# Kernel optimization log

Measured on AMD Instinct MI355X. Metric: run time of the kernel, lower is better.

## Reference

```python
import jax, jax.numpy as jnp
import numpy as np

B, L, N, F = 8, 4096, 128, 128          # batch, pixels (64x64), memories, filters
H, DK, DV = 8, 16, 32                   # heads, key dim/head, value dim/head
TK, TV = H * DK, H * DV                 # total key depth 128, total value depth 256
BOT, FFN = 256, 2048                    # bottleneck (2*filters), feed-forward channels
EPS = 1e-3                              # keras BatchNormalization epsilon
INV = float(1.0 / np.sqrt(1.0 + EPS))   # inference BN with moving mean=0, var=1


def _bn_pair(k, shape):
    kg, kb = jax.random.split(k)
    gamma = jax.random.uniform(kg, shape, jnp.float32, 0.5, 1.5)
    beta = 0.1 * jax.random.normal(kb, shape, jnp.float32)
    return jnp.stack([gamma, beta])


def setup_inputs() -> dict:
    key = jax.random.key(0)
    ks = jax.random.split(key, 24)
    s = float(BOT) ** -0.5  # TruncatedNormal(stddev=bottleneck**-0.5) init for qkv convs
    return {
        "pixel_input": jax.random.normal(ks[0], (B, L, F), jnp.float32),
        "memory_input": jax.random.normal(ks[1], (B, N, F), jnp.float32),
        "W_mem1": 0.05 * jax.random.normal(ks[2], (F, BOT), jnp.float32),
        "bn_mem1": _bn_pair(ks[3], (BOT,)),
        "W_pix1": 0.05 * jax.random.normal(ks[4], (F, BOT), jnp.float32),
        "bn_pix1": _bn_pair(ks[5], (BOT,)),
        "W_mem_qkv": s * jax.random.normal(ks[6], (BOT, 2 * TK + TV), jnp.float32),
        "bn_mem_qkv": _bn_pair(ks[7], (2 * TK + TV,)),
        "W_pix_qkv": s * jax.random.normal(ks[8], (BOT, 2 * TK + TV), jnp.float32),
        "bn_pix_qkv": _bn_pair(ks[9], (2 * TK + TV,)),
        "bn_mem_sim": _bn_pair(ks[10], (H,)),
        "bn_mem_ret": _bn_pair(ks[11], (H, DV)),
        "bn_pix_sim": _bn_pair(ks[12], (H,)),
        "bn_pix_ret": _bn_pair(ks[13], (H, DV)),
        "W_mem3": 0.05 * jax.random.normal(ks[14], (TV, F), jnp.float32),
        "bn_mem3": _bn_pair(ks[15], (F,)),
        "W_pix3": 0.05 * jax.random.normal(ks[16], (TV, F), jnp.float32),
        "bn_pix3": _bn_pair(ks[17], (F,)),
        "W_ffn1": 0.05 * jax.random.normal(ks[18], (F, FFN), jnp.float32),
        "bn_ffn1": _bn_pair(ks[19], (FFN,)),
        "W_ffn2": 0.05 * jax.random.normal(ks[20], (FFN, F), jnp.float32),
        "bn_ffn2": _bn_pair(ks[21], (F,)),
    }


def _cbn(x, W, p, relu=False):
    """Conv1D (kernel=1) + inference BatchNorm over channels (+ optional relu)."""
    y = jnp.einsum('blc,cd->bld', x, W)
    y = y * (p[0] * INV) + p[1]
    return jax.nn.relu(y) if relu else y


def _heads(t, d):
    b, l, _ = t.shape  # [b, l, H*d] -> [b, H, l, d]
    return t.reshape(b, l, H, d).transpose(0, 2, 1, 3)


def reference(pixel_input, memory_input, W_mem1, bn_mem1, W_pix1, bn_pix1,
              W_mem_qkv, bn_mem_qkv, W_pix_qkv, bn_pix_qkv,
              bn_mem_sim, bn_mem_ret, bn_pix_sim, bn_pix_ret,
              W_mem3, bn_mem3, W_pix3, bn_pix3,
              W_ffn1, bn_ffn1, W_ffn2, bn_ffn2):
    # Bottleneck projections (conv1 + BN + relu)
    mem = _cbn(memory_input, W_mem1, bn_mem1, True)   # [B, N, BOT]
    pix = _cbn(pixel_input, W_pix1, bn_pix1, True)    # [B, L, BOT]

    # QKV projections (conv + BN, no activation)
    mqkv = _cbn(mem, W_mem_qkv, bn_mem_qkv)           # [B, N, 2*TK+TV]
    pqkv = _cbn(pix, W_pix_qkv, bn_pix_qkv)           # [B, L, 2*TK+TV]
    mq, mk, mv = mqkv[..., :TK], mqkv[..., TK:2 * TK], mqkv[..., 2 * TK:]
    pq, pk, pv = pqkv[..., :TK], pqkv[..., TK:2 * TK], pqkv[..., 2 * TK:]
    mq_h, mk_h = _heads(mq, DK), _heads(mk, DK)       # [B, H, N, DK]
    pq_h, pk_h = _heads(pq, DK), _heads(pk, DK)       # [B, H, L, DK]
    mv_h = mv.reshape(B, N, H, DV)                    # [B, N, H, DV]
    pv_h = pv.reshape(B, L, H, DV)                    # [B, L, H, DV]

    # Memory path: memory2pixel attention + memory self-attention share softmax
    k_cat = jnp.concatenate([pk_h, mk_h], axis=2)     # [B, H, L+N, DK]
    v_cat = jnp.concatenate([pv_h, mv_h], axis=1)     # [B, L+N, H, DV]
    logits = jnp.einsum('bhnd,bhmd->bhnm', mq_h, k_cat)
    logits = logits * (bn_mem_sim[0] * INV)[None, :, None, None] + bn_mem_sim[1][None, :, None, None]
    attn = jax.nn.softmax(logits, axis=-1)
    ret = jnp.einsum('bhnm,bmhd->bhnd', attn, v_cat)  # [B, H, N, DV]
    ret = ret * (bn_mem_ret[0] * INV)[None, :, None, :] + bn_mem_ret[1][None, :, None, :]
    ret = jax.nn.relu(ret).transpose(0, 2, 1, 3).reshape(B, N, TV)
    mem_out = jax.nn.relu(memory_input + _cbn(ret, W_mem3, bn_mem3))
    ffn = _cbn(mem_out, W_ffn1, bn_ffn1, True)
    mem_out = jax.nn.relu(mem_out + _cbn(ffn, W_ffn2, bn_ffn2))

    # Pixel path: pixel2memory feedback attention (sigmoid activation)
    plogits = jnp.einsum('bhld,bhnd->bhln', pq_h, mk_h)
    plogits = plogits * (bn_pix_sim[0] * INV)[None, :, None, None] + bn_pix_sim[1][None, :, None, None]
    pattn = jax.nn.sigmoid(plogits)
    pret = jnp.einsum('bhln,bnhd->bhld', pattn, mv_h)  # [B, H, L, DV]
    pret = pret * (bn_pix_ret[0] * INV)[None, :, None, :] + bn_pix_ret[1][None, :, None, :]
    pret = jax.nn.relu(pret).transpose(0, 2, 1, 3).reshape(B, L, TV)
    pix_out = jax.nn.relu(pixel_input + _cbn(pret, W_pix3, bn_pix3))

    return pix_out, mem_out
```

## Files before the change

### kernel.cpp

```cpp
#include <hip/hip_runtime.h>

typedef __attribute__((ext_vector_type(8))) short short8;
typedef __attribute__((ext_vector_type(4))) float floatx4;

#define INVC 0.9995003746877732f
#define MSPLIT 8

__device__ __forceinline__ unsigned short f2bf(float f) {
    union { float f; unsigned int u; } c; c.f = f;
    unsigned int r = c.u + 0x7fffu + ((c.u >> 16) & 1u);
    return (unsigned short)(r >> 16);
}
__device__ __forceinline__ float bf2f(unsigned short u) {
    union { unsigned int u; float f; } c; c.u = ((unsigned int)u) << 16;
    return c.f;
}
__device__ __forceinline__ void gld_lds16(const unsigned short* g, unsigned short* l) {
    __builtin_amdgcn_global_load_lds(
        (const __attribute__((address_space(1))) unsigned int*)g,
        (__attribute__((address_space(3))) unsigned int*)l, 16, 0, 0);
}
__device__ __forceinline__ int fidx(int row, int k) {
    return (k >> 5) * 512 + (row + 16 * ((k >> 3) & 3)) * 8 + (k & 7);
}

struct PrepPtrs {
    const float* src_pix;
    unsigned short* dst_pix;
    const float* W[8]; unsigned short* Wt[8];
};

__global__ __launch_bounds__(256) void prep_kernel(PrepPtrs P) {
    __shared__ float T[32][33];
    const int bid = blockIdx.x, t = threadIdx.x;
    if (bid < 4096) {
        int i = bid * 1024 + t * 4;
        float4 v = *(const float4*)(P.src_pix + i);
        unsigned long long pk = (unsigned long long)f2bf(v.x)
            | ((unsigned long long)f2bf(v.y) << 16)
            | ((unsigned long long)f2bf(v.z) << 32)
            | ((unsigned long long)f2bf(v.w) << 48);
        *(unsigned long long*)(P.dst_pix + i) = pk;
        return;
    }
    int rel = bid - 4096;
    const int KD[8]  = {128,128,256,256,256,256,128,2048};
    const int ND[8]  = {256,256,512,512,128,128,2048,128};
    const int CNT[8] = {32,32,128,128,32,32,256,256};
    int wi = 0;
    #pragma unroll
    for (int k = 0; k < 8; ++k) { if (rel >= CNT[k] && wi == k) { rel -= CNT[k]; wi = k + 1; } }
    const int K = KD[wi], N = ND[wi];
    const int ntn = N >> 5;
    const int tn = rel % ntn, tk = rel / ntn;
    const int n0 = tn * 32, k0 = tk * 32;
    const float* W = P.W[wi];
    unsigned short* Wt = P.Wt[wi];
    const int tx = t & 31, ty = t >> 5;
    #pragma unroll
    for (int i = 0; i < 4; ++i)
        T[ty + 8*i][tx] = W[(size_t)(k0 + ty + 8*i) * N + n0 + tx];
    __syncthreads();
    #pragma unroll
    for (int i = 0; i < 4; ++i)
        Wt[(size_t)(n0 + ty + 8*i) * K + k0 + tx] = f2bf(T[tx][ty + 8*i]);
}

__global__ __launch_bounds__(256, 4) void gemm_bf16(
    const unsigned short* __restrict__ A,
    const unsigned short* __restrict__ Bt,
    const float* __restrict__ bnp,
    const float* __restrict__ residF,
    unsigned short* __restrict__ outB,
    float* __restrict__ outF,
    int M, int K, int Nc, int do_relu)
{
    __shared__ unsigned short As[8 * 512];
    __shared__ unsigned short Bs[8 * 512];
    const int t = threadIdx.x;
    const int lane = t & 63, w = t >> 6;
    const int l15 = lane & 15, quad = lane >> 4;
    const int wr = w >> 1, wc = w & 1;
    const int row0 = blockIdx.y * 128;
    const int col0 = blockIdx.x * 128;

    floatx4 acc[4][4];
    #pragma unroll
    for (int i = 0; i < 4; ++i)
        #pragma unroll
        for (int j = 0; j < 4; ++j) acc[i][j] = (floatx4){0.f, 0.f, 0.f, 0.f};

    const unsigned short* gA0 = A  + (size_t)(row0 + w*16     + l15) * K + quad*8;
    const unsigned short* gA1 = A  + (size_t)(row0 + (w+4)*16 + l15) * K + quad*8;
    const unsigned short* gB0 = Bt + (size_t)(col0 + w*16     + l15) * K + quad*8;
    const unsigned short* gB1 = Bt + (size_t)(col0 + (w+4)*16 + l15) * K + quad*8;
    unsigned short* lA0 = &As[w * 512];
    unsigned short* lA1 = &As[(w + 4) * 512];
    unsigned short* lB0 = &Bs[w * 512];
    unsigned short* lB1 = &Bs[(w + 4) * 512];

    for (int k0 = 0; k0 < K; k0 += 32) {
        __syncthreads();
        gld_lds16(gA0 + k0, lA0);
        gld_lds16(gA1 + k0, lA1);
        gld_lds16(gB0 + k0, lB0);
        gld_lds16(gB1 + k0, lB1);
        __syncthreads();
        short8 a[4], b[4];
        #pragma unroll
        for (int mt = 0; mt < 4; ++mt) a[mt] = *(const short8*)&As[(wr*4 + mt)*512 + lane*8];
        #pragma unroll
        for (int nt = 0; nt < 4; ++nt) b[nt] = *(const short8*)&Bs[(wc*4 + nt)*512 + lane*8];
        #pragma unroll
        for (int mt = 0; mt < 4; ++mt)
            #pragma unroll
            for (int nt = 0; nt < 4; ++nt)
                acc[mt][nt] = __builtin_amdgcn_mfma_f32_16x16x32_bf16(a[mt], b[nt], acc[mt][nt], 0, 0, 0);
    }

    #pragma unroll
    for (int mt = 0; mt < 4; ++mt) {
        const int rowb = row0 + wr*64 + mt*16 + quad*4;
        #pragma unroll
        for (int nt = 0; nt < 4; ++nt) {
            const int col = col0 + wc*64 + nt*16 + l15;
            floatx4 v = acc[mt][nt];
            const float g  = bnp[col] * INVC;
            const float be = bnp[Nc + col];
            #pragma unroll
            for (int r = 0; r < 4; ++r) {
                size_t off = (size_t)(rowb + r) * Nc + col;
                float v1 = v[r] * g + be;
                if (residF) v1 += residF[off];
                if (do_relu) v1 = fmaxf(v1, 0.f);
                if (outB) outB[off] = f2bf(v1);
                if (outF) outF[off] = v1;
            }
        }
    }
}

__global__ __launch_bounds__(256) void mem_fused(
    const float* __restrict__ memory_input,
    const unsigned short* __restrict__ Wt0, const float* __restrict__ bn1,
    const unsigned short* __restrict__ Wt2, const float* __restrict__ bnq,
    unsigned short* __restrict__ mqkv)
{
    __shared__ unsigned short A0[4*512];
    __shared__ unsigned short A1[8*512];
    const int t = threadIdx.x;
    const int lane = t & 63, w = t >> 6;
    const int l15 = lane & 15, quad = lane >> 4;
    const int g0 = blockIdx.x * 16;

    {
        const int row = t >> 4;
        const int c0 = (t & 15) * 8;
        const float* src = memory_input + (size_t)(g0 + row) * 128 + c0;
        float4 v0 = *(const float4*)src;
        float4 v1 = *(const float4*)(src + 4);
        float vv[8] = {v0.x, v0.y, v0.z, v0.w, v1.x, v1.y, v1.z, v1.w};
        #pragma unroll
        for (int e = 0; e < 8; ++e)
            A0[fidx(row, c0 + e)] = f2bf(vv[e]);
    }
    __syncthreads();

    #pragma unroll
    for (int i = 0; i < 4; ++i) {
        const int n0 = (w*4 + i) * 16;
        floatx4 acc = {0.f,0.f,0.f,0.f};
        #pragma unroll
        for (int kc = 0; kc < 4; ++kc) {
            short8 a = *(const short8*)&A0[kc*512 + lane*8];
            short8 bfr = *(const short8*)&Wt0[(size_t)(n0 + l15)*128 + kc*32 + quad*8];
            acc = __builtin_amdgcn_mfma_f32_16x16x32_bf16(a, bfr, acc, 0, 0, 0);
        }
        const int col = n0 + l15;
        const float g = bn1[col] * INVC, be = bn1[256 + col];
        #pragma unroll
        for (int r = 0; r < 4; ++r) {
            const int row = quad*4 + r;
            float v = fmaxf(acc[r]*g + be, 0.f);
            A1[fidx(row, col)] = f2bf(v);
        }
    }
    __syncthreads();

    #pragma unroll
    for (int i = 0; i < 8; ++i) {
        const int n0 = w*128 + i*16;
        floatx4 acc = {0.f,0.f,0.f,0.f};
        #pragma unroll
        for (int kc = 0; kc < 8; ++kc) {
            short8 a = *(const short8*)&A1[kc*512 + lane*8];
            short8 bfr = *(const short8*)&Wt2[(size_t)(n0 + l15)*256 + kc*32 + quad*8];
            acc = __builtin_amdgcn_mfma_f32_16x16x32_bf16(a, bfr, acc, 0, 0, 0);
        }
        const int col = n0 + l15;
        const float g = bnq[col] * INVC, be = bnq[512 + col];
        #pragma unroll
        for (int r = 0; r < 4; ++r) {
            const int row = quad*4 + r;
            mqkv[(size_t)(g0 + row)*512 + col] = f2bf(acc[r]*g + be);
        }
    }
}

__global__ __launch_bounds__(256) void ffn_fused(
    const float* __restrict__ part_acc, const float* __restrict__ part_ml,
    const float* __restrict__ bn_ret,
    const unsigned short* __restrict__ Wt4, const float* __restrict__ bn3,
    const float* __restrict__ memory_input,
    const unsigned short* __restrict__ Wt6, const float* __restrict__ bnf1,
    const unsigned short* __restrict__ Wt7, const float* __restrict__ bnf2,
    float* __restrict__ out_mem)
{
    __shared__ unsigned short mretA[8*512];
    __shared__ unsigned short moA[4*512];
    __shared__ unsigned short fA[64*512];
    const int t = threadIdx.x;
    const int lane = t & 63, w = t >> 6;
    const int l15 = lane & 15, quad = lane >> 4;
    const int g0 = blockIdx.x * 16;
    const int b = g0 >> 7;
    const int nbase = g0 & 127;

    {
        const int row = t >> 4;
        const int c0 = (t & 15) * 16;
        const int h = c0 >> 5;
        const int n = nbase + row;
        const int bh = b*8 + h;
        float ms[MSPLIT], ls[MSPLIT], m_g = -1e30f;
        #pragma unroll
        for (int s = 0; s < MSPLIT; ++s) {
            size_t o = ((size_t)(bh*MSPLIT + s)*128 + n)*2;
            ms[s] = part_ml[o]; ls[s] = part_ml[o+1];
            m_g = fmaxf(m_g, ms[s]);
        }
        float l_g = 0.f;
        float og[16];
        #pragma unroll
        for (int e = 0; e < 16; ++e) og[e] = 0.f;
        #pragma unroll
        for (int s = 0; s < MSPLIT; ++s) {
            float wgt = __expf(ms[s] - m_g);
            l_g += ls[s] * wgt;
            const float* pa = part_acc + ((size_t)(bh*MSPLIT + s)*128 + n)*32 + (c0 & 31);
            #pragma unroll
            for (int e = 0; e < 16; e += 4) {
                float4 v = *(const float4*)(pa + e);
                og[e]   += v.x*wgt; og[e+1] += v.y*wgt;
                og[e+2] += v.z*wgt; og[e+3] += v.w*wgt;
            }
        }
        float invl = 1.f / l_g;
        #pragma unroll
        for (int e = 0; e < 16; ++e) {
            int col = c0 + e;
            int dv = col & 31;
            float v = og[e]*invl*(bn_ret[h*32+dv]*INVC) + bn_ret[256 + h*32 + dv];
            mretA[fidx(row, col)] = f2bf(fmaxf(v, 0.f));
        }
    }
    __syncthreads();

    floatx4 mo[2];
    #pragma unroll
    for (int i = 0; i < 2; ++i) {
        const int n0 = (w*2 + i) * 16;
        floatx4 acc = {0.f,0.f,0.f,0.f};
        #pragma unroll
        for (int kc = 0; kc < 8; ++kc) {
            short8 a = *(const short8*)&mretA[kc*512 + lane*8];
            short8 bfr = *(const short8*)&Wt4[(size_t)(n0 + l15)*256 + kc*32 + quad*8];
            acc = __builtin_amdgcn_mfma_f32_16x16x32_bf16(a, bfr, acc, 0, 0, 0);
        }
        const int col = n0 + l15;
        const float g = bn3[col]*INVC, be = bn3[128 + col];
        #pragma unroll
        for (int r = 0; r < 4; ++r) {
            const int row = quad*4 + r;
            float v = acc[r]*g + be + memory_input[(size_t)(g0 + row)*128 + col];
            v = fmaxf(v, 0.f);
            mo[i][r] = v;
            moA[fidx(row, col)] = f2bf(v);
        }
    }
    __syncthreads();

    for (int nt = 0; nt < 32; ++nt) {
        const int n0 = w*512 + nt*16;
        floatx4 acc = {0.f,0.f,0.f,0.f};
        #pragma unroll
        for (int kc = 0; kc < 4; ++kc) {
            short8 a = *(const short8*)&moA[kc*512 + lane*8];
            short8 bfr = *(const short8*)&Wt6[(size_t)(n0 + l15)*128 + kc*32 + quad*8];
            acc = __builtin_amdgcn_mfma_f32_16x16x32_bf16(a, bfr, acc, 0, 0, 0);
        }
        const int col = n0 + l15;
        const float g = bnf1[col]*INVC, be = bnf1[2048 + col];
        #pragma unroll
        for (int r = 0; r < 4; ++r) {
            const int row = quad*4 + r;
            fA[fidx(row, col)] = f2bf(fmaxf(acc[r]*g + be, 0.f));
        }
    }
    __syncthreads();

    #pragma unroll
    for (int i = 0; i < 2; ++i) {
        const int n0 = (w*2 + i) * 16;
        floatx4 acc = {0.f,0.f,0.f,0.f};
        #pragma unroll 8
        for (int kc = 0; kc < 64; ++kc) {
            short8 a = *(const short8*)&fA[kc*512 + lane*8];
            short8 bfr = *(const short8*)&Wt7[(size_t)(n0 + l15)*2048 + kc*32 + quad*8];
            acc = __builtin_amdgcn_mfma_f32_16x16x32_bf16(a, bfr, acc, 0, 0, 0);
        }
        const int col = n0 + l15;
        const float g = bnf2[col]*INVC, be = bnf2[128 + col];
        #pragma unroll
        for (int r = 0; r < 4; ++r) {
            const int row = quad*4 + r;
            float v = fmaxf(acc[r]*g + be + mo[i][r], 0.f);
            out_mem[(size_t)(g0 + row)*128 + col] = v;
        }
    }
}

__global__ __launch_bounds__(256) void pix_attn(
    const unsigned short* __restrict__ pqkv,
    const unsigned short* __restrict__ mqkv,
    const float* __restrict__ bn_sim,
    const float* __restrict__ bn_ret,
    unsigned short* __restrict__ pret)
{
    __shared__ unsigned short Qs[128][40];
    __shared__ unsigned short Ks[128][40];
    __shared__ unsigned short VsT[32][136];
    __shared__ unsigned short Ps[128][136];
    const int t = threadIdx.x;
    const int lane = t & 63, w = t >> 6;
    const int l15 = lane & 15, quad = lane >> 4;
    const int bx = blockIdx.x;
    const int lt = bx & 31, h = (bx >> 5) & 7, b = bx >> 8;
    const int l0 = lt * 128;
    const float simg = bn_sim[h] * INVC, simb = bn_sim[8 + h];

    {
        const int r = t >> 1, half = t & 1;
        uint4 zz = make_uint4(0u, 0u, 0u, 0u);
        const unsigned short* qsrc = pqkv + ((size_t)(b*4096 + l0 + r) << 9) + h*16 + half*8;
        *(uint4*)&Qs[r][half*8] = *(const uint4*)qsrc;
        *(uint4*)&Qs[r][16 + half*8] = zz;
        const unsigned short* ksrc = mqkv + ((size_t)(b*128 + r) << 9) + 128 + h*16 + half*8;
        *(uint4*)&Ks[r][half*8] = *(const uint4*)ksrc;
        *(uint4*)&Ks[r][16 + half*8] = zz;
        const unsigned short* vsrc = mqkv + ((size_t)(b*128 + r) << 9) + 256 + h*32 + half*16;
        uint4 va = *(const uint4*)vsrc;
        uint4 vb = *(const uint4*)(vsrc + 8);
        const int d0 = half * 16;
        VsT[d0+0][r] = (unsigned short)(va.x & 0xffffu); VsT[d0+1][r] = (unsigned short)(va.x >> 16);
        VsT[d0+2][r] = (unsigned short)(va.y & 0xffffu); VsT[d0+3][r] = (unsigned short)(va.y >> 16);
        VsT[d0+4][r] = (unsigned short)(va.z & 0xffffu); VsT[d0+5][r] = (unsigned short)(va.z >> 16);
        VsT[d0+6][r] = (unsigned short)(va.w & 0xffffu); VsT[d0+7][r] = (unsigned short)(va.w >> 16);
        VsT[d0+8][r] = (unsigned short)(vb.x & 0xffffu); VsT[d0+9][r] = (unsigned short)(vb.x >> 16);
        VsT[d0+10][r] = (unsigned short)(vb.y & 0xffffu); VsT[d0+11][r] = (unsigned short)(vb.y >> 16);
        VsT[d0+12][r] = (unsigned short)(vb.z & 0xffffu); VsT[d0+13][r] = (unsigned short)(vb.z >> 16);
        VsT[d0+14][r] = (unsigned short)(vb.w & 0xffffu); VsT[d0+15][r] = (unsigned short)(vb.w >> 16);
    }
    __syncthreads();

    floatx4 z4 = {0.f, 0.f, 0.f, 0.f};
    #pragma unroll
    for (int half = 0; half < 2; ++half) {
        short8 aq = *(const short8*)&Qs[w*32 + half*16 + l15][quad*8];
        #pragma unroll
        for (int nt = 0; nt < 8; ++nt) {
            short8 bk = *(const short8*)&Ks[nt*16 + l15][quad*8];
            floatx4 s = __builtin_amdgcn_mfma_f32_16x16x32_bf16(aq, bk, z4, 0, 0, 0);
            const int rowb = w*32 + half*16 + quad*4;
            #pragma unroll
            for (int r = 0; r < 4; ++r) {
                float x = s[r] * simg + simb;
                float p = 1.f / (1.f + __expf(-x));
                Ps[rowb + r][nt*16 + l15] = f2bf(p);
            }
        }
    }
    __syncthreads();

    #pragma unroll
    for (int half = 0; half < 2; ++half) {
        const int mrow = w*32 + half*16;
        #pragma unroll
        for (int dvt = 0; dvt < 2; ++dvt) {
            floatx4 acc = {0.f, 0.f, 0.f, 0.f};
            #pragma unroll
            for (int ks = 0; ks < 4; ++ks) {
                short8 ap = *(const short8*)&Ps[mrow + l15][ks*32 + quad*8];
                short8 bv = *(const short8*)&VsT[dvt*16 + l15][ks*32 + quad*8];
                acc = __builtin_amdgcn_mfma_f32_16x16x32_bf16(ap, bv, acc, 0, 0, 0);
            }
            const int dv = dvt*16 + l15;
            const float g  = bn_ret[h*32 + dv] * INVC;
            const float be = bn_ret[256 + h*32 + dv];
            #pragma unroll
            for (int r = 0; r < 4; ++r) {
                const int row = l0 + mrow + quad*4 + r;
                float v = fmaxf(acc[r] * g + be, 0.f);
                pret[((size_t)(b*4096 + row) << 8) + h*32 + dv] = f2bf(v);
            }
        }
    }
}

__global__ __launch_bounds__(256) void mem_attn(
    const unsigned short* __restrict__ mqkv,
    const unsigned short* __restrict__ pqkv,
    const float* __restrict__ bn_sim,
    float* __restrict__ part_acc,
    float* __restrict__ part_ml)
{
    __shared__ unsigned short Qs[128][40];
    __shared__ unsigned short Ks[128][40];
    __shared__ unsigned short VsT[32][136];
    __shared__ unsigned short Ps[128][136];
    const int t = threadIdx.x;
    const int lane = t & 63, w = t >> 6;
    const int l15 = lane & 15, quad = lane >> 4;
    const int bx = blockIdx.x;
    const int s = bx & (MSPLIT-1), h = (bx >> 3) & 7, b = bx >> 6;
    const int bh = b*8 + h;
    const float simg = bn_sim[h] * INVC, simb = bn_sim[8 + h];
    const int c0  = (s == 0) ? 0 : (4*s + 1);
    const int cnt = (s == 0) ? 5 : 4;

    {
        const int r = t >> 1, half = t & 1;
        uint4 zz = make_uint4(0u, 0u, 0u, 0u);
        const unsigned short* qsrc = mqkv + ((size_t)(b*128 + r) << 9) + h*16 + half*8;
        *(uint4*)&Qs[r][half*8] = *(const uint4*)qsrc;
        *(uint4*)&Qs[r][16 + half*8] = zz;
    }

    float m_run[2][4], l_run[2][4];
    floatx4 accpv[2][2];
    #pragma unroll
    for (int i = 0; i < 2; ++i) {
        #pragma unroll
        for (int r = 0; r < 4; ++r) { m_run[i][r] = -1e30f; l_run[i][r] = 0.f; }
        accpv[i][0] = (floatx4){0.f,0.f,0.f,0.f};
        accpv[i][1] = (floatx4){0.f,0.f,0.f,0.f};
    }
    floatx4 z4 = {0.f, 0.f, 0.f, 0.f};

    for (int ci = 0; ci < cnt; ++ci) {
        const int c = c0 + ci;
        __syncthreads();
        {
            const int r = t >> 1, half = t & 1;
            uint4 zz = make_uint4(0u, 0u, 0u, 0u);
            const unsigned short* base = (c < 32)
                ? (pqkv + ((size_t)(b*4096 + c*128 + r) << 9))
                : (mqkv + ((size_t)(b*128 + r) << 9));
            *(uint4*)&Ks[r][half*8] = *(const uint4*)(base + 128 + h*16 + half*8);
            *(uint4*)&Ks[r][16 + half*8] = zz;
            const unsigned short* vsrc = base + 256 + h*32 + half*16;
            uint4 va = *(const uint4*)vsrc;
            uint4 vb = *(const uint4*)(vsrc + 8);
            const int d0 = half * 16;
            VsT[d0+0][r] = (unsigned short)(va.x & 0xffffu); VsT[d0+1][r] = (unsigned short)(va.x >> 16);
            VsT[d0+2][r] = (unsigned short)(va.y & 0xffffu); VsT[d0+3][r] = (unsigned short)(va.y >> 16);
            VsT[d0+4][r] = (unsigned short)(va.z & 0xffffu); VsT[d0+5][r] = (unsigned short)(va.z >> 16);
            VsT[d0+6][r] = (unsigned short)(va.w & 0xffffu); VsT[d0+7][r] = (unsigned short)(va.w >> 16);
            VsT[d0+8][r] = (unsigned short)(vb.x & 0xffffu); VsT[d0+9][r] = (unsigned short)(vb.x >> 16);
            VsT[d0+10][r] = (unsigned short)(vb.y & 0xffffu); VsT[d0+11][r] = (unsigned short)(vb.y >> 16);
            VsT[d0+12][r] = (unsigned short)(vb.z & 0xffffu); VsT[d0+13][r] = (unsigned short)(vb.z >> 16);
            VsT[d0+14][r] = (unsigned short)(vb.w & 0xffffu); VsT[d0+15][r] = (unsigned short)(vb.w >> 16);
        }
        __syncthreads();

        #pragma unroll
        for (int half = 0; half < 2; ++half) {
            float sv[8][4];
            short8 aq = *(const short8*)&Qs[w*32 + half*16 + l15][quad*8];
            #pragma unroll
            for (int nt = 0; nt < 8; ++nt) {
                short8 bk = *(const short8*)&Ks[nt*16 + l15][quad*8];
                floatx4 sr4 = __builtin_amdgcn_mfma_f32_16x16x32_bf16(aq, bk, z4, 0, 0, 0);
                #pragma unroll
                for (int r = 0; r < 4; ++r) sv[nt][r] = sr4[r] * simg + simb;
            }
            const int rowb = w*32 + half*16 + quad*4;
            #pragma unroll
            for (int r = 0; r < 4; ++r) {
                float mx = sv[0][r];
                #pragma unroll
                for (int nt = 1; nt < 8; ++nt) mx = fmaxf(mx, sv[nt][r]);
                mx = fmaxf(mx, __shfl_xor(mx, 1));
                mx = fmaxf(mx, __shfl_xor(mx, 2));
                mx = fmaxf(mx, __shfl_xor(mx, 4));
                mx = fmaxf(mx, __shfl_xor(mx, 8));
                float newm  = fmaxf(m_run[half][r], mx);
                float alpha = __expf(m_run[half][r] - newm);
                m_run[half][r] = newm;
                float lsum = 0.f;
                #pragma unroll
                for (int nt = 0; nt < 8; ++nt) {
                    float p = __expf(sv[nt][r] - newm);
                    lsum += p;
                    Ps[rowb + r][nt*16 + l15] = f2bf(p);
                }
                lsum += __shfl_xor(lsum, 1);
                lsum += __shfl_xor(lsum, 2);
                lsum += __shfl_xor(lsum, 4);
                lsum += __shfl_xor(lsum, 8);
                l_run[half][r] = l_run[half][r] * alpha + lsum;
                accpv[half][0][r] *= alpha;
                accpv[half][1][r] *= alpha;
            }
            __syncthreads();
            const int mrow = w*32 + half*16;
            #pragma unroll
            for (int dvt = 0; dvt < 2; ++dvt) {
                floatx4 a = accpv[half][dvt];
                #pragma unroll
                for (int ks = 0; ks < 4; ++ks) {
                    short8 ap = *(const short8*)&Ps[mrow + l15][ks*32 + quad*8];
                    short8 bv = *(const short8*)&VsT[dvt*16 + l15][ks*32 + quad*8];
                    a = __builtin_amdgcn_mfma_f32_16x16x32_bf16(ap, bv, a, 0, 0, 0);
                }
                accpv[half][dvt] = a;
            }
        }
    }

    #pragma unroll
    for (int half = 0; half < 2; ++half) {
        const int rowb = w*32 + half*16 + quad*4;
        #pragma unroll
        for (int dvt = 0; dvt < 2; ++dvt) {
            const int dv = dvt*16 + l15;
            #pragma unroll
            for (int r = 0; r < 4; ++r)
                part_acc[((size_t)(bh*MSPLIT + s)*128 + rowb + r)*32 + dv] = accpv[half][dvt][r];
        }
        if (l15 == 0) {
            #pragma unroll
            for (int r = 0; r < 4; ++r) {
                size_t o = ((size_t)(bh*MSPLIT + s)*128 + rowb + r) * 2;
                part_ml[o]     = m_run[half][r];
                part_ml[o + 1] = l_run[half][r];
            }
        }
    }
}

extern "C" void kernel_launch(void* const* d_in, const int* in_sizes, int n_in,
                              void* d_out, int out_size, void* d_ws, size_t ws_size,
                              hipStream_t stream) {
    const float* pixel_input  = (const float*)d_in[0];
    const float* memory_input = (const float*)d_in[1];
    const float* W_mem1    = (const float*)d_in[2];
    const float* bn_mem1   = (const float*)d_in[3];
    const float* W_pix1    = (const float*)d_in[4];
    const float* bn_pix1   = (const float*)d_in[5];
    const float* W_mem_qkv = (const float*)d_in[6];
    const float* bn_mem_qkv= (const float*)d_in[7];
    const float* W_pix_qkv = (const float*)d_in[8];
    const float* bn_pix_qkv= (const float*)d_in[9];
    const float* bn_mem_sim= (const float*)d_in[10];
    const float* bn_mem_ret= (const float*)d_in[11];
    const float* bn_pix_sim= (const float*)d_in[12];
    const float* bn_pix_ret= (const float*)d_in[13];
    const float* W_mem3    = (const float*)d_in[14];
    const float* bn_mem3   = (const float*)d_in[15];
    const float* W_pix3    = (const float*)d_in[16];
    const float* bn_pix3   = (const float*)d_in[17];
    const float* W_ffn1    = (const float*)d_in[18];
    const float* bn_ffn1   = (const float*)d_in[19];
    const float* W_ffn2    = (const float*)d_in[20];
    const float* bn_ffn2   = (const float*)d_in[21];

    char* ws = (char*)d_ws;
    size_t off = 0;
    auto alloc = [&](size_t bytes) -> void* {
        void* p = ws + off; off += (bytes + 255) & ~(size_t)255; return p;
    };
    unsigned short* pixB  = (unsigned short*)alloc((size_t)32768*128*2);
    unsigned short* Wt0   = (unsigned short*)alloc((size_t)256*128*2);
    unsigned short* Wt1   = (unsigned short*)alloc((size_t)256*128*2);
    unsigned short* Wt2   = (unsigned short*)alloc((size_t)512*256*2);
    unsigned short* Wt3   = (unsigned short*)alloc((size_t)512*256*2);
    unsigned short* Wt4   = (unsigned short*)alloc((size_t)128*256*2);
    unsigned short* Wt5   = (unsigned short*)alloc((size_t)128*256*2);
    unsigned short* Wt6   = (unsigned short*)alloc((size_t)2048*128*2);
    unsigned short* Wt7   = (unsigned short*)alloc((size_t)128*2048*2);
    unsigned short* mqkvB = (unsigned short*)alloc((size_t)1024*512*2);
    unsigned short* pixA  = (unsigned short*)alloc((size_t)32768*256*2);
    unsigned short* pqkvB = (unsigned short*)alloc((size_t)32768*512*2);
    float* part_acc = (float*)alloc((size_t)64*MSPLIT*128*32*4);
    float* part_ml  = (float*)alloc((size_t)64*MSPLIT*128*2*4);
    unsigned short* pretB = (unsigned short*)alloc((size_t)32768*256*2);

    float* out_pix = (float*)d_out;
    float* out_mem = (float*)d_out + (size_t)8*4096*128;

    PrepPtrs P;
    P.src_pix = pixel_input;
    P.dst_pix = pixB;
    P.W[0]=W_mem1; P.W[1]=W_pix1; P.W[2]=W_mem_qkv; P.W[3]=W_pix_qkv;
    P.W[4]=W_mem3; P.W[5]=W_pix3; P.W[6]=W_ffn1;    P.W[7]=W_ffn2;
    P.Wt[0]=Wt0; P.Wt[1]=Wt1; P.Wt[2]=Wt2; P.Wt[3]=Wt3;
    P.Wt[4]=Wt4; P.Wt[5]=Wt5; P.Wt[6]=Wt6; P.Wt[7]=Wt7;

    dim3 blk(256);
    prep_kernel<<<4992, blk, 0, stream>>>(P);

    gemm_bf16<<<dim3(2,256,1), blk, 0, stream>>>(pixB, Wt1, bn_pix1, nullptr,
        pixA, nullptr, 32768, 128, 256, 1);
    gemm_bf16<<<dim3(4,256,1), blk, 0, stream>>>(pixA, Wt3, bn_pix_qkv, nullptr,
        pqkvB, nullptr, 32768, 256, 512, 0);
    mem_fused<<<64, blk, 0, stream>>>(memory_input, Wt0, bn_mem1, Wt2, bn_mem_qkv, mqkvB);

    mem_attn<<<64*MSPLIT, blk, 0, stream>>>(mqkvB, pqkvB, bn_mem_sim, part_acc, part_ml);

    ffn_fused<<<64, blk, 0, stream>>>(part_acc, part_ml, bn_mem_ret,
        Wt4, bn_mem3, memory_input, Wt6, bn_ffn1, Wt7, bn_ffn2, out_mem);

    pix_attn<<<2048, blk, 0, stream>>>(pqkvB, mqkvB, bn_pix_sim, bn_pix_ret, pretB);
    gemm_bf16<<<dim3(1,256,1), blk, 0, stream>>>(pretB, Wt5, bn_pix3, pixel_input,
        nullptr, out_pix, 32768, 256, 128, 1);
}
```

Measured before the change: 283.7 us.

## Merge independent kernels into shared launches and widen FFN block to 1024 threads

Independent stages are packed into single launches that branch on block index: pix1 GEMM with the memory QKV path, pixel and memory attention together, and the pix3 GEMM with the memory attention combine and mem3 projection. The FFN moves into its own kernel with 1024 threads that split the second GEMM's K dimension across two groups and reduce through shared memory. The aim is fewer launches and better overlap, since the small 64-block memory kernels otherwise leave most of the GPU idle. In exchange there is an extra bf16 round trip for the memory output, the residual is now rounded to bf16, and the FFN still runs serially at the end.

New measurement: 262.8 us. 1.08x faster.

```diff
diff --git a/kernel.cpp b/kernel.cpp
--- a/kernel.cpp
+++ b/kernel.cpp
@@ -66,23 +66,20 @@
         Wt[(size_t)(n0 + ty + 8*i) * K + k0 + tx] = f2bf(T[tx][ty + 8*i]);
 }
 
-__global__ __launch_bounds__(256, 4) void gemm_bf16(
+__device__ __forceinline__ void gemm_body(
     const unsigned short* __restrict__ A,
     const unsigned short* __restrict__ Bt,
     const float* __restrict__ bnp,
     const float* __restrict__ residF,
     unsigned short* __restrict__ outB,
     float* __restrict__ outF,
-    int M, int K, int Nc, int do_relu)
+    int K, int Nc, int do_relu, int row0, int col0,
+    unsigned short* As, unsigned short* Bs)
 {
-    __shared__ unsigned short As[8 * 512];
-    __shared__ unsigned short Bs[8 * 512];
     const int t = threadIdx.x;
     const int lane = t & 63, w = t >> 6;
     const int l15 = lane & 15, quad = lane >> 4;
     const int wr = w >> 1, wc = w & 1;
-    const int row0 = blockIdx.y * 128;
-    const int col0 = blockIdx.x * 128;
 
     floatx4 acc[4][4];
     #pragma unroll
@@ -140,18 +137,39 @@
     }
 }
 
-__global__ __launch_bounds__(256) void mem_fused(
+__global__ __launch_bounds__(256, 4) void gemm_bf16(
+    const unsigned short* __restrict__ A, const unsigned short* __restrict__ Bt,
+    const float* __restrict__ bnp, unsigned short* __restrict__ outB,
+    int K, int Nc)
+{
+    __shared__ unsigned short As[8 * 512];
+    __shared__ unsigned short Bs[8 * 512];
+    gemm_body(A, Bt, bnp, nullptr, outB, nullptr, K, Nc, 0,
+              blockIdx.y * 128, blockIdx.x * 128, As, Bs);
+}
+
+__global__ __launch_bounds__(256) void k_pix1_memfused(
+    const unsigned short* __restrict__ pixB, const unsigned short* __restrict__ Wt1,
+    const float* __restrict__ bn_pix1, unsigned short* __restrict__ pixA,
     const float* __restrict__ memory_input,
     const unsigned short* __restrict__ Wt0, const float* __restrict__ bn1,
     const unsigned short* __restrict__ Wt2, const float* __restrict__ bnq,
     unsigned short* __restrict__ mqkv)
 {
-    __shared__ unsigned short A0[4*512];
-    __shared__ unsigned short A1[8*512];
+    __shared__ unsigned short As[8 * 512];
+    __shared__ unsigned short Bs[8 * 512];
+    const int bx = blockIdx.x;
+    if (bx < 512) {
+        gemm_body(pixB, Wt1, bn_pix1, nullptr, pixA, nullptr, 128, 256, 1,
+                  (bx >> 1) * 128, (bx & 1) * 128, As, Bs);
+        return;
+    }
+    unsigned short* A0 = As;
+    unsigned short* A1 = Bs;
     const int t = threadIdx.x;
     const int lane = t & 63, w = t >> 6;
     const int l15 = lane & 15, quad = lane >> 4;
-    const int g0 = blockIdx.x * 16;
+    const int g0 = (bx - 512) * 16;
 
     {
         const int row = t >> 4;
@@ -207,135 +225,13 @@
     }
 }
 
-__global__ __launch_bounds__(256) void ffn_fused(
-    const float* __restrict__ part_acc, const float* __restrict__ part_ml,
-    const float* __restrict__ bn_ret,
-    const unsigned short* __restrict__ Wt4, const float* __restrict__ bn3,
-    const float* __restrict__ memory_input,
-    const unsigned short* __restrict__ Wt6, const float* __restrict__ bnf1,
-    const unsigned short* __restrict__ Wt7, const float* __restrict__ bnf2,
-    float* __restrict__ out_mem)
-{
-    __shared__ unsigned short mretA[8*512];
-    __shared__ unsigned short moA[4*512];
-    __shared__ unsigned short fA[64*512];
-    const int t = threadIdx.x;
-    const int lane = t & 63, w = t >> 6;
-    const int l15 = lane & 15, quad = lane >> 4;
-    const int g0 = blockIdx.x * 16;
-    const int b = g0 >> 7;
-    const int nbase = g0 & 127;
-
-    {
-        const int row = t >> 4;
-        const int c0 = (t & 15) * 16;
-        const int h = c0 >> 5;
-        const int n = nbase + row;
-        const int bh = b*8 + h;
-        float ms[MSPLIT], ls[MSPLIT], m_g = -1e30f;
-        #pragma unroll
-        for (int s = 0; s < MSPLIT; ++s) {
-            size_t o = ((size_t)(bh*MSPLIT + s)*128 + n)*2;
-            ms[s] = part_ml[o]; ls[s] = part_ml[o+1];
-            m_g = fmaxf(m_g, ms[s]);
-        }
-        float l_g = 0.f;
-        float og[16];
-        #pragma unroll
-        for (int e = 0; e < 16; ++e) og[e] = 0.f;
-        #pragma unroll
-        for (int s = 0; s < MSPLIT; ++s) {
-            float wgt = __expf(ms[s] - m_g);
-            l_g += ls[s] * wgt;
-            const float* pa = part_acc + ((size_t)(bh*MSPLIT + s)*128 + n)*32 + (c0 & 31);
-            #pragma unroll
-            for (int e = 0; e < 16; e += 4) {
-                float4 v = *(const float4*)(pa + e);
-                og[e]   += v.x*wgt; og[e+1] += v.y*wgt;
-                og[e+2] += v.z*wgt; og[e+3] += v.w*wgt;
-            }
-        }
-        float invl = 1.f / l_g;
-        #pragma unroll
-        for (int e = 0; e < 16; ++e) {
-            int col = c0 + e;
-            int dv = col & 31;
-            float v = og[e]*invl*(bn_ret[h*32+dv]*INVC) + bn_ret[256 + h*32 + dv];
-            mretA[fidx(row, col)] = f2bf(fmaxf(v, 0.f));
-        }
-    }
-    __syncthreads();
-
-    floatx4 mo[2];
-    #pragma unroll
-    for (int i = 0; i < 2; ++i) {
-        const int n0 = (w*2 + i) * 16;
-        floatx4 acc = {0.f,0.f,0.f,0.f};
-        #pragma unroll
-        for (int kc = 0; kc < 8; ++kc) {
-            short8 a = *(const short8*)&mretA[kc*512 + lane*8];
-            short8 bfr = *(const short8*)&Wt4[(size_t)(n0 + l15)*256 + kc*32 + quad*8];
-            acc = __builtin_amdgcn_mfma_f32_16x16x32_bf16(a, bfr, acc, 0, 0, 0);
-        }
-        const int col = n0 + l15;
-        const float g = bn3[col]*INVC, be = bn3[128 + col];
-        #pragma unroll
-        for (int r = 0; r < 4; ++r) {
-            const int row = quad*4 + r;
-            float v = acc[r]*g + be + memory_input[(size_t)(g0 + row)*128 + col];
-            v = fmaxf(v, 0.f);
-            mo[i][r] = v;
-            moA[fidx(row, col)] = f2bf(v);
-        }
-    }
-    __syncthreads();
-
-    for (int nt = 0; nt < 32; ++nt) {
-        const int n0 = w*512 + nt*16;
-        floatx4 acc = {0.f,0.f,0.f,0.f};
-        #pragma unroll
-        for (int kc = 0; kc < 4; ++kc) {
-            short8 a = *(const short8*)&moA[kc*512 + lane*8];
-            short8 bfr = *(const short8*)&Wt6[(size_t)(n0 + l15)*128 + kc*32 + quad*8];
-            acc = __builtin_amdgcn_mfma_f32_16x16x32_bf16(a, bfr, acc, 0, 0, 0);
-        }
-        const int col = n0 + l15;
-        const float g = bnf1[col]*INVC, be = bnf1[2048 + col];
-        #pragma unroll
-        for (int r = 0; r < 4; ++r) {
-            const int row = quad*4 + r;
-            fA[fidx(row, col)] = f2bf(fmaxf(acc[r]*g + be, 0.f));
-        }
-    }
-    __syncthreads();
-
-    #pragma unroll
-    for (int i = 0; i < 2; ++i) {
-        const int n0 = (w*2 + i) * 16;
-        floatx4 acc = {0.f,0.f,0.f,0.f};
-        #pragma unroll 8
-        for (int kc = 0; kc < 64; ++kc) {
-            short8 a = *(const short8*)&fA[kc*512 + lane*8];
-            short8 bfr = *(const short8*)&Wt7[(size_t)(n0 + l15)*2048 + kc*32 + quad*8];
-            acc = __builtin_amdgcn_mfma_f32_16x16x32_bf16(a, bfr, acc, 0, 0, 0);
-        }
-        const int col = n0 + l15;
-        const float g = bnf2[col]*INVC, be = bnf2[128 + col];
-        #pragma unroll
-        for (int r = 0; r < 4; ++r) {
-            const int row = quad*4 + r;
-            float v = fmaxf(acc[r]*g + be + mo[i][r], 0.f);
-            out_mem[(size_t)(g0 + row)*128 + col] = v;
-        }
-    }
-}
-
-__global__ __launch_bounds__(256) void pix_attn(
+__global__ __launch_bounds__(256) void k_attn(
     const unsigned short* __restrict__ pqkv,
     const unsigned short* __restrict__ mqkv,
-    const float* __restrict__ bn_sim,
-    const float* __restrict__ bn_ret,
-    unsigned short* __restrict__ pret)
+    const float* __restrict__ bn_psim, const float* __restrict__ bn_pret,
+    unsigned short* __restrict__ pret,
+    const float* __restrict__ bn_msim,
+    float* __restrict__ part_acc, float* __restrict__ part_ml)
 {
     __shared__ unsigned short Qs[128][40];
     __shared__ unsigned short Ks[128][40];
@@ -344,97 +240,83 @@
     const int t = threadIdx.x;
     const int lane = t & 63, w = t >> 6;
     const int l15 = lane & 15, quad = lane >> 4;
-    const int bx = blockIdx.x;
-    const int lt = bx & 31, h = (bx >> 5) & 7, b = bx >> 8;
-    const int l0 = lt * 128;
-    const float simg = bn_sim[h] * INVC, simb = bn_sim[8 + h];
-
-    {
-        const int r = t >> 1, half = t & 1;
-        uint4 zz = make_uint4(0u, 0u, 0u, 0u);
-        const unsigned short* qsrc = pqkv + ((size_t)(b*4096 + l0 + r) << 9) + h*16 + half*8;
-        *(uint4*)&Qs[r][half*8] = *(const uint4*)qsrc;
-        *(uint4*)&Qs[r][16 + half*8] = zz;
-        const unsigned short* ksrc = mqkv + ((size_t)(b*128 + r) << 9) + 128 + h*16 + half*8;
-        *(uint4*)&Ks[r][half*8] = *(const uint4*)ksrc;
-        *(uint4*)&Ks[r][16 + half*8] = zz;
-        const unsigned short* vsrc = mqkv + ((size_t)(b*128 + r) << 9) + 256 + h*32 + half*16;
-        uint4 va = *(const uint4*)vsrc;
-        uint4 vb = *(const uint4*)(vsrc + 8);
-        const int d0 = half * 16;
-        VsT[d0+0][r] = (unsigned short)(va.x & 0xffffu); VsT[d0+1][r] = (unsigned short)(va.x >> 16);
-        VsT[d0+2][r] = (unsigned short)(va.y & 0xffffu); VsT[d0+3][r] = (unsigned short)(va.y >> 16);
-        VsT[d0+4][r] = (unsigned short)(va.z & 0xffffu); VsT[d0+5][r] = (unsigned short)(va.z >> 16);
-        VsT[d0+6][r] = (unsigned short)(va.w & 0xffffu); VsT[d0+7][r] = (unsigned short)(va.w >> 16);
-        VsT[d0+8][r] = (unsigned short)(vb.x & 0xffffu); VsT[d0+9][r] = (unsigned short)(vb.x >> 16);
-        VsT[d0+10][r] = (unsigned short)(vb.y & 0xffffu); VsT[d0+11][r] = (unsigned short)(vb.y >> 16);
-        VsT[d0+12][r] = (unsigned short)(vb.z & 0xffffu); VsT[d0+13][r] = (unsigned short)(vb.z >> 16);
-        VsT[d0+14][r] = (unsigned short)(vb.w & 0xffffu); VsT[d0+15][r] = (unsigned short)(vb.w >> 16);
-    }
-    __syncthreads();
-
     floatx4 z4 = {0.f, 0.f, 0.f, 0.f};
-    #pragma unroll
-    for (int half = 0; half < 2; ++half) {
-        short8 aq = *(const short8*)&Qs[w*32 + half*16 + l15][quad*8];
-        #pragma unroll
-        for (int nt = 0; nt < 8; ++nt) {
-            short8 bk = *(const short8*)&Ks[nt*16 + l15][quad*8];
-            floatx4 s = __builtin_amdgcn_mfma_f32_16x16x32_bf16(aq, bk, z4, 0, 0, 0);
-            const int rowb = w*32 + half*16 + quad*4;
-            #pragma unroll
-            for (int r = 0; r < 4; ++r) {
-                float x = s[r] * simg + simb;
-                float p = 1.f / (1.f + __expf(-x));
-                Ps[rowb + r][nt*16 + l15] = f2bf(p);
-            }
-        }
-    }
-    __syncthreads();
-
-    #pragma unroll
-    for (int half = 0; half < 2; ++half) {
-        const int mrow = w*32 + half*16;
-        #pragma unroll
-        for (int dvt = 0; dvt < 2; ++dvt) {
-            floatx4 acc = {0.f, 0.f, 0.f, 0.f};
-            #pragma unroll
-            for (int ks = 0; ks < 4; ++ks) {
-                short8 ap = *(const short8*)&Ps[mrow + l15][ks*32 + quad*8];
-                short8 bv = *(const short8*)&VsT[dvt*16 + l15][ks*32 + quad*8];
-                acc = __builtin_amdgcn_mfma_f32_16x16x32_bf16(ap, bv, acc, 0, 0, 0);
-            }
-            const int dv = dvt*16 + l15;
-            const float g  = bn_ret[h*32 + dv] * INVC;
-            const float be = bn_ret[256 + h*32 + dv];
-            #pragma unroll
-            for (int r = 0; r < 4; ++r) {
-                const int row = l0 + mrow + quad*4 + r;
-                float v = fmaxf(acc[r] * g + be, 0.f);
-                pret[((size_t)(b*4096 + row) << 8) + h*32 + dv] = f2bf(v);
-            }
-        }
-    }
-}
-
-__global__ __launch_bounds__(256) void mem_attn(
-    const unsigned short* __restrict__ mqkv,
-    const unsigned short* __restrict__ pqkv,
-    const float* __restrict__ bn_sim,
-    float* __restrict__ part_acc,
-    float* __restrict__ part_ml)
-{
-    __shared__ unsigned short Qs[128][40];
-    __shared__ unsigned short Ks[128][40];
-    __shared__ unsigned short VsT[32][136];
-    __shared__ unsigned short Ps[128][136];
-    const int t = threadIdx.x;
-    const int lane = t & 63, w = t >> 6;
-    const int l15 = lane & 15, quad = lane >> 4;
-    const int bx = blockIdx.x;
-    const int s = bx & (MSPLIT-1), h = (bx >> 3) & 7, b = bx >> 6;
+
+    if (blockIdx.x < 2048) {
+        const int bx = blockIdx.x;
+        const int lt = bx & 31, h = (bx >> 5) & 7, b = bx >> 8;
+        const int l0 = lt * 128;
+        const float simg = bn_psim[h] * INVC, simb = bn_psim[8 + h];
+        {
+            const int r = t >> 1, half = t & 1;
+            uint4 zz = make_uint4(0u, 0u, 0u, 0u);
+            const unsigned short* qsrc = pqkv + ((size_t)(b*4096 + l0 + r) << 9) + h*16 + half*8;
+            *(uint4*)&Qs[r][half*8] = *(const uint4*)qsrc;
+            *(uint4*)&Qs[r][16 + half*8] = zz;
+            const unsigned short* ksrc = mqkv + ((size_t)(b*128 + r) << 9) + 128 + h*16 + half*8;
+            *(uint4*)&Ks[r][half*8] = *(const uint4*)ksrc;
+            *(uint4*)&Ks[r][16 + half*8] = zz;
+            const unsigned short* vsrc = mqkv + ((size_t)(b*128 + r) << 9) + 256 + h*32 + half*16;
+            uint4 va = *(const uint4*)vsrc;
+            uint4 vb = *(const uint4*)(vsrc + 8);
+            const int d0 = half * 16;
+            VsT[d0+0][r] = (unsigned short)(va.x & 0xffffu); VsT[d0+1][r] = (unsigned short)(va.x >> 16);
+            VsT[d0+2][r] = (unsigned short)(va.y & 0xffffu); VsT[d0+3][r] = (unsigned short)(va.y >> 16);
+            VsT[d0+4][r] = (unsigned short)(va.z & 0xffffu); VsT[d0+5][r] = (unsigned short)(va.z >> 16);
+            VsT[d0+6][r] = (unsigned short)(va.w & 0xffffu); VsT[d0+7][r] = (unsigned short)(va.w >> 16);
+            VsT[d0+8][r] = (unsigned short)(vb.x & 0xffffu); VsT[d0+9][r] = (unsigned short)(vb.x >> 16);
+            VsT[d0+10][r] = (unsigned short)(vb.y & 0xffffu); VsT[d0+11][r] = (unsigned short)(vb.y >> 16);
+            VsT[d0+12][r] = (unsigned short)(vb.z & 0xffffu); VsT[d0+13][r] = (unsigned short)(vb.z >> 16);
+            VsT[d0+14][r] = (unsigned short)(vb.w & 0xffffu); VsT[d0+15][r] = (unsigned short)(vb.w >> 16);
+        }
+        __syncthreads();
+        #pragma unroll
+        for (int half = 0; half < 2; ++half) {
+            short8 aq = *(const short8*)&Qs[w*32 + half*16 + l15][quad*8];
+            #pragma unroll
+            for (int nt = 0; nt < 8; ++nt) {
+                short8 bk = *(const short8*)&Ks[nt*16 + l15][quad*8];
+                floatx4 s = __builtin_amdgcn_mfma_f32_16x16x32_bf16(aq, bk, z4, 0, 0, 0);
+                const int rowb = w*32 + half*16 + quad*4;
+                #pragma unroll
+                for (int r = 0; r < 4; ++r) {
+                    float x = s[r] * simg + simb;
+                    float p = 1.f / (1.f + __expf(-x));
+                    Ps[rowb + r][nt*16 + l15] = f2bf(p);
+                }
+            }
+        }
+        __syncthreads();
+        #pragma unroll
+        for (int half = 0; half < 2; ++half) {
+            const int mrow = w*32 + half*16;
+            #pragma unroll
+            for (int dvt = 0; dvt < 2; ++dvt) {
+                floatx4 acc = {0.f, 0.f, 0.f, 0.f};
+                #pragma unroll
+                for (int ks = 0; ks < 4; ++ks) {
+                    short8 ap = *(const short8*)&Ps[mrow + l15][ks*32 + quad*8];
+                    short8 bv = *(const short8*)&VsT[dvt*16 + l15][ks*32 + quad*8];
+                    acc = __builtin_amdgcn_mfma_f32_16x16x32_bf16(ap, bv, acc, 0, 0, 0);
+                }
+                const int dv = dvt*16 + l15;
+                const float g  = bn_pret[h*32 + dv] * INVC;
+                const float be = bn_pret[256 + h*32 + dv];
+                #pragma unroll
+                for (int r = 0; r < 4; ++r) {
+                    const int row = l0 + mrow + quad*4 + r;
+                    float v = fmaxf(acc[r] * g + be, 0.f);
+                    pret[((size_t)(b*4096 + row) << 8) + h*32 + dv] = f2bf(v);
+                }
+            }
+        }
+        return;
+    }
+
+    const int bxm = blockIdx.x - 2048;
+    const int s = bxm & (MSPLIT-1), h = (bxm >> 3) & 7, b = bxm >> 6;
     const int bh = b*8 + h;
-    const float simg = bn_sim[h] * INVC, simb = bn_sim[8 + h];
+    const float simg = bn_msim[h] * INVC, simb = bn_msim[8 + h];
     const int c0  = (s == 0) ? 0 : (4*s + 1);
     const int cnt = (s == 0) ? 5 : 4;
 
@@ -455,7 +337,6 @@
         accpv[i][0] = (floatx4){0.f,0.f,0.f,0.f};
         accpv[i][1] = (floatx4){0.f,0.f,0.f,0.f};
     }
-    floatx4 z4 = {0.f, 0.f, 0.f, 0.f};
 
     for (int ci = 0; ci < cnt; ++ci) {
         const int c = c0 + ci;
@@ -559,6 +440,170 @@
     }
 }
 
+__global__ __launch_bounds__(256) void k_pix3_combmem3(
+    const unsigned short* __restrict__ pretB, const unsigned short* __restrict__ Wt5,
+    const float* __restrict__ bn_pix3, const float* __restrict__ pixel_input,
+    float* __restrict__ out_pix,
+    const float* __restrict__ part_acc, const float* __restrict__ part_ml,
+    const float* __restrict__ bn_ret,
+    const unsigned short* __restrict__ Wt4, const float* __restrict__ bn3,
+    const float* __restrict__ memory_input,
+    unsigned short* __restrict__ moB)
+{
+    __shared__ unsigned short As[8 * 512];
+    __shared__ unsigned short Bs[8 * 512];
+    const int bx = blockIdx.x;
+    if (bx < 256) {
+        gemm_body(pretB, Wt5, bn_pix3, pixel_input, nullptr, out_pix, 256, 128, 1,
+                  bx * 128, 0, As, Bs);
+        return;
+    }
+    unsigned short* mretA = As;
+    const int t = threadIdx.x;
+    const int lane = t & 63, w = t >> 6;
+    const int l15 = lane & 15, quad = lane >> 4;
+    const int g0 = (bx - 256) * 16;
+    const int b = g0 >> 7;
+    const int nbase = g0 & 127;
+
+    {
+        const int row = t >> 4;
+        const int c0 = (t & 15) * 16;
+        const int h = c0 >> 5;
+        const int n = nbase + row;
+        const int bh = b*8 + h;
+        float ms[MSPLIT], ls[MSPLIT], m_g = -1e30f;
+        #pragma unroll
+        for (int s = 0; s < MSPLIT; ++s) {
+            size_t o = ((size_t)(bh*MSPLIT + s)*128 + n)*2;
+            ms[s] = part_ml[o]; ls[s] = part_ml[o+1];
+            m_g = fmaxf(m_g, ms[s]);
+        }
+        float l_g = 0.f;
+        float og[16];
+        #pragma unroll
+        for (int e = 0; e < 16; ++e) og[e] = 0.f;
+        #pragma unroll
+        for (int s = 0; s < MSPLIT; ++s) {
+            float wgt = __expf(ms[s] - m_g);
+            l_g += ls[s] * wgt;
+            const float* pa = part_acc + ((size_t)(bh*MSPLIT + s)*128 + n)*32 + (c0 & 31);
+            #pragma unroll
+            for (int e = 0; e < 16; e += 4) {
+                float4 v = *(const float4*)(pa + e);
+                og[e]   += v.x*wgt; og[e+1] += v.y*wgt;
+                og[e+2] += v.z*wgt; og[e+3] += v.w*wgt;
+            }
+        }
+        float invl = 1.f / l_g;
+        #pragma unroll
+        for (int e = 0; e < 16; ++e) {
+            int col = c0 + e;
+            int dv = col & 31;
+            float v = og[e]*invl*(bn_ret[h*32+dv]*INVC) + bn_ret[256 + h*32 + dv];
+            mretA[fidx(row, col)] = f2bf(fmaxf(v, 0.f));
+        }
+    }
+    __syncthreads();
+
+    #pragma unroll
+    for (int i = 0; i < 2; ++i) {
+        const int n0 = (w*2 + i) * 16;
+        floatx4 acc = {0.f,0.f,0.f,0.f};
+        #pragma unroll
+        for (int kc = 0; kc < 8; ++kc) {
+            short8 a = *(const short8*)&mretA[kc*512 + lane*8];
+            short8 bfr = *(const short8*)&Wt4[(size_t)(n0 + l15)*256 + kc*32 + quad*8];
+            acc = __builtin_amdgcn_mfma_f32_16x16x32_bf16(a, bfr, acc, 0, 0, 0);
+        }
+        const int col = n0 + l15;
+        const float g = bn3[col]*INVC, be = bn3[128 + col];
+        #pragma unroll
+        for (int r = 0; r < 4; ++r) {
+            const int row = quad*4 + r;
+            float v = acc[r]*g + be + memory_input[(size_t)(g0 + row)*128 + col];
+            moB[(size_t)(g0 + row)*128 + col] = f2bf(fmaxf(v, 0.f));
+        }
+    }
+}
+
+__global__ __launch_bounds__(1024) void k_ffn(
+    const unsigned short* __restrict__ moB,
+    const unsigned short* __restrict__ Wt6, const float* __restrict__ bnf1,
+    const unsigned short* __restrict__ Wt7, const float* __restrict__ bnf2,
+    float* __restrict__ out_mem)
+{
+    __shared__ unsigned short moA[4*512];
+    __shared__ unsigned short fA[64*512];
+    __shared__ floatx4 red[2][8][64];
+    const int t = threadIdx.x;
+    const int lane = t & 63, w = t >> 6;
+    const int l15 = lane & 15, quad = lane >> 4;
+    const int g0 = blockIdx.x * 16;
+
+    if (t < 256) {
+        const int row = t >> 4;
+        const int c0 = (t & 15) * 8;
+        uint4 v = *(const uint4*)(moB + (size_t)(g0 + row)*128 + c0);
+        unsigned short e0 = (unsigned short)(v.x & 0xffffu), e1 = (unsigned short)(v.x >> 16);
+        unsigned short e2 = (unsigned short)(v.y & 0xffffu), e3 = (unsigned short)(v.y >> 16);
+        unsigned short e4 = (unsigned short)(v.z & 0xffffu), e5 = (unsigned short)(v.z >> 16);
+        unsigned short e6 = (unsigned short)(v.w & 0xffffu), e7 = (unsigned short)(v.w >> 16);
+        moA[fidx(row, c0+0)] = e0; moA[fidx(row, c0+1)] = e1;
+        moA[fidx(row, c0+2)] = e2; moA[fidx(row, c0+3)] = e3;
+        moA[fidx(row, c0+4)] = e4; moA[fidx(row, c0+5)] = e5;
+        moA[fidx(row, c0+6)] = e6; moA[fidx(row, c0+7)] = e7;
+    }
+    __syncthreads();
+
+    #pragma unroll
+    for (int i = 0; i < 8; ++i) {
+        const int n0 = (w*8 + i) * 16;
+        floatx4 acc = {0.f,0.f,0.f,0.f};
+        #pragma unroll
+        for (int kc = 0; kc < 4; ++kc) {
+            short8 a = *(const short8*)&moA[kc*512 + lane*8];
+            short8 bfr = *(const short8*)&Wt6[(size_t)(n0 + l15)*128 + kc*32 + quad*8];
+            acc = __builtin_amdgcn_mfma_f32_16x16x32_bf16(a, bfr, acc, 0, 0, 0);
+        }
+        const int col = n0 + l15;
+        const float g = bnf1[col]*INVC, be = bnf1[2048 + col];
+        #pragma unroll
+        for (int r = 0; r < 4; ++r)
+            fA[fidx(quad*4 + r, col)] = f2bf(fmaxf(acc[r]*g + be, 0.f));
+    }
+    __syncthreads();
+
+    {
+        const int ntile = w & 7, khalf = w >> 3;
+        const int n0 = ntile * 16;
+        floatx4 acc = {0.f,0.f,0.f,0.f};
+        #pragma unroll 8
+        for (int kc = 0; kc < 32; ++kc) {
+            const int kcu = khalf*32 + kc;
+            short8 a = *(const short8*)&fA[kcu*512 + lane*8];
+            short8 bfr = *(const short8*)&Wt7[(size_t)(n0 + l15)*2048 + kcu*32 + quad*8];
+            acc = __builtin_amdgcn_mfma_f32_16x16x32_bf16(a, bfr, acc, 0, 0, 0);
+        }
+        red[khalf][ntile][lane] = acc;
+    }
+    __syncthreads();
+    if (w < 8) {
+        const int n0 = w * 16;
+        floatx4 s0 = red[0][w][lane];
+        floatx4 s1 = red[1][w][lane];
+        const int col = n0 + l15;
+        const float g = bnf2[col]*INVC, be = bnf2[128 + col];
+        #pragma unroll
+        for (int r = 0; r < 4; ++r) {
+            const int row = quad*4 + r;
+            float resid = bf2f(moA[fidx(row, col)]);
+            float v = fmaxf((s0[r] + s1[r])*g + be + resid, 0.f);
+            out_mem[(size_t)(g0 + row)*128 + col] = v;
+        }
+    }
+}
+
 extern "C" void kernel_launch(void* const* d_in, const int* in_sizes, int n_in,
                               void* d_out, int out_size, void* d_ws, size_t ws_size,
                               hipStream_t stream) {
@@ -605,6 +650,7 @@
     float* part_acc = (float*)alloc((size_t)64*MSPLIT*128*32*4);
     float* part_ml  = (float*)alloc((size_t)64*MSPLIT*128*2*4);
     unsigned short* pretB = (unsigned short*)alloc((size_t)32768*256*2);
+    unsigned short* moB   = (unsigned short*)alloc((size_t)1024*128*2);
 
     float* out_pix = (float*)d_out;
     float* out_mem = (float*)d_out + (size_t)8*4096*128;
@@ -619,19 +665,12 @@
 
     dim3 blk(256);
     prep_kernel<<<4992, blk, 0, stream>>>(P);
-
-    gemm_bf16<<<dim3(2,256,1), blk, 0, stream>>>(pixB, Wt1, bn_pix1, nullptr,
-        pixA, nullptr, 32768, 128, 256, 1);
-    gemm_bf16<<<dim3(4,256,1), blk, 0, stream>>>(pixA, Wt3, bn_pix_qkv, nullptr,
-        pqkvB, nullptr, 32768, 256, 512, 0);
-    mem_fused<<<64, blk, 0, stream>>>(memory_input, Wt0, bn_mem1, Wt2, bn_mem_qkv, mqkvB);
-
-    mem_attn<<<64*MSPLIT, blk, 0, stream>>>(mqkvB, pqkvB, bn_mem_sim, part_acc, part_ml);
-
-    ffn_fused<<<64, blk, 0, stream>>>(part_acc, part_ml, bn_mem_ret,
-        Wt4, bn_mem3, memory_input, Wt6, bn_ffn1, Wt7, bn_ffn2, out_mem);
-
-    pix_attn<<<2048, blk, 0, stream>>>(pqkvB, mqkvB, bn_pix_sim, bn_pix_ret, pretB);
-    gemm_bf16<<<dim3(1,256,1), blk, 0, stream>>>(pretB, Wt5, bn_pix3, pixel_input,
-        nullptr, out_pix, 32768, 256, 128, 1);
-}
+    k_pix1_memfused<<<576, blk, 0, stream>>>(pixB, Wt1, bn_pix1, pixA,
+        memory_input, Wt0, bn_mem1, Wt2, bn_mem_qkv, mqkvB);
+    gemm_bf16<<<dim3(4,256,1), blk, 0, stream>>>(pixA, Wt3, bn_pix_qkv, pqkvB, 256, 512);
+    k_attn<<<2048 + 64*MSPLIT, blk, 0, stream>>>(pqkvB, mqkvB,
+        bn_pix_sim, bn_pix_ret, pretB, bn_mem_sim, part_acc, part_ml);
+    k_pix3_combmem3<<<320, blk, 0, stream>>>(pretB, Wt5, bn_pix3, pixel_input, out_pix,
+        part_acc, part_ml, bn_mem_ret, Wt4, bn_mem3, memory_input, moB);
+    k_ffn<<<64, dim3(1024), 0, stream>>>(moB, Wt6, bn_ffn1, Wt7, bn_ffn2, out_mem);
+}
```
